# Performance work log

Measured on AMD Instinct MI355X. Metric: run time of the kernel, lower is better.

## Reference

```python
import jax, jax.numpy as jnp
import numpy as np

NUM_BINS = 8
TAIL = 3.0
MIN_W = 1e-3
MIN_H = 1e-3
MIN_D = 1e-3


def setup_inputs() -> dict:
    key = jax.random.key(0)
    k1, k2 = jax.random.split(key)
    inputs = jax.random.normal(k1, (8192, 2048), dtype=jnp.float32)
    params = 0.01 * jax.random.normal(k2, (2048, NUM_BINS * 3 - 1), dtype=jnp.float32)
    return {"inputs": inputs, "params": params}


def _rqs(inputs, params):
    # inputs: (B, D); params: (D, 3K-1). Each dim has its own spline (no coupling).
    K = NUM_BINS
    D = params.shape[0]
    uw = params[:, :K]
    uh = params[:, K:2 * K]
    ud = params[:, 2 * K:]  # (D, K-1)

    # pad edge derivatives so that softplus(const) = 1 - min_derivative (linear tails)
    const = float(np.log(np.exp(1.0 - MIN_D) - 1.0))
    ud = jnp.pad(ud, ((0, 0), (1, 1)), constant_values=const)  # (D, K+1)

    widths = MIN_W + (1.0 - MIN_W * K) * jax.nn.softmax(uw, axis=-1)
    cw = jnp.pad(jnp.cumsum(widths, axis=-1), ((0, 0), (1, 0)))  # (D, K+1) in [0,1]
    cw = (2.0 * TAIL) * cw - TAIL
    cw = cw.at[:, 0].set(-TAIL).at[:, -1].set(TAIL)
    widths = cw[:, 1:] - cw[:, :-1]

    heights = MIN_H + (1.0 - MIN_H * K) * jax.nn.softmax(uh, axis=-1)
    ch = jnp.pad(jnp.cumsum(heights, axis=-1), ((0, 0), (1, 0)))
    ch = (2.0 * TAIL) * ch - TAIL
    ch = ch.at[:, 0].set(-TAIL).at[:, -1].set(TAIL)
    heights = ch[:, 1:] - ch[:, :-1]

    derivs = MIN_D + jax.nn.softplus(ud)  # (D, K+1)

    inside = (inputs >= -TAIL) & (inputs <= TAIL)
    x = jnp.clip(inputs, -TAIL, TAIL)

    # searchsorted per element: bin index in [0, K-1], shape (B, D)
    idx = jnp.clip(jnp.sum((x[..., None] >= cw[None, :, :]).astype(jnp.int32), axis=-1) - 1, 0, K - 1)
    d_idx = jnp.arange(D)[None, :]  # broadcasts with (B, D) idx

    icw = cw[d_idx, idx]
    iw = widths[d_idx, idx]
    ich = ch[d_idx, idx]
    ih = heights[d_idx, idx]
    dlo = derivs[d_idx, idx]
    dhi = derivs[d_idx, idx + 1]

    delta = ih / iw
    theta = (x - icw) / iw
    t1m = theta * (1.0 - theta)

    numerator = ih * (delta * theta ** 2 + dlo * t1m)
    denominator = delta + (dlo + dhi - 2.0 * delta) * t1m
    out = ich + numerator / denominator

    deriv_num = delta ** 2 * (dhi * theta ** 2 + 2.0 * delta * t1m + dlo * (1.0 - theta) ** 2)
    logdet = jnp.log(deriv_num) - 2.0 * jnp.log(denominator)

    out = jnp.where(inside, out, inputs)     # identity tails
    logdet = jnp.where(inside, logdet, 0.0)
    return out, logdet


def reference(inputs, params):
    return _rqs(inputs, params)
```

## Files before the change

### kernel.cpp

```cpp
#include <hip/hip_runtime.h>


constexpr int   KBINS = 8;
constexpr float TAILF = 3.0f;
constexpr float MINW  = 0.001f;
constexpr float MINH  = 0.001f;
constexpr float MIND  = 0.001f;
constexpr int   NROWS = 8192;
constexpr int   NDIM  = 2048;
constexpr int   NPAR  = 3 * KBINS - 1;
constexpr int   VEC   = 2;
constexpr int   BLOCK = 256;
constexpr int   DIMS_PER_BLOCK = BLOCK * VEC;
constexpr int   BLOCKS_PER_ROW = NDIM / DIMS_PER_BLOCK;
constexpr int   GROWS = 512;
constexpr int   ROWS_PER_WALK = NROWS / GROWS;

typedef float v2f __attribute__((ext_vector_type(2)));

__device__ __forceinline__ float rcp_fast(float x) {
    return __builtin_amdgcn_rcpf(x);
}

__device__ __forceinline__ float softplus_fast(float x) {
    return fmaxf(x, 0.0f) + __logf(1.0f + __expf(-fabsf(x)));
}

__device__ __forceinline__ void build_tables(const float* __restrict__ p,
                                             float* cw, float* ch, float* dv,
                                             float edge_deriv) {
    {
        float u[KBINS];
        float m = p[0];
#pragma unroll
        for (int k = 1; k < KBINS; ++k) m = fmaxf(m, p[k]);
        float s = 0.0f;
#pragma unroll
        for (int k = 0; k < KBINS; ++k) { u[k] = __expf(p[k] - m); s += u[k]; }
        const float scale = (1.0f - MINW * KBINS) * rcp_fast(s);
        cw[0] = -TAILF;
        float acc = 0.0f;
#pragma unroll
        for (int k = 0; k < KBINS; ++k) {
            acc += MINW + scale * u[k];
            cw[k + 1] = fmaf(2.0f * TAILF, acc, -TAILF);
        }
        cw[KBINS] = TAILF;
    }
    {
        const float* q = p + KBINS;
        float u[KBINS];
        float m = q[0];
#pragma unroll
        for (int k = 1; k < KBINS; ++k) m = fmaxf(m, q[k]);
        float s = 0.0f;
#pragma unroll
        for (int k = 0; k < KBINS; ++k) { u[k] = __expf(q[k] - m); s += u[k]; }
        const float scale = (1.0f - MINH * KBINS) * rcp_fast(s);
        ch[0] = -TAILF;
        float acc = 0.0f;
#pragma unroll
        for (int k = 0; k < KBINS; ++k) {
            acc += MINH + scale * u[k];
            ch[k + 1] = fmaf(2.0f * TAILF, acc, -TAILF);
        }
        ch[KBINS] = TAILF;
    }
    dv[0] = edge_deriv;
    dv[KBINS] = edge_deriv;
#pragma unroll
    for (int k = 1; k < KBINS; ++k)
        dv[k] = MIND + softplus_fast(p[2 * KBINS + k - 1]);
}

__device__ __forceinline__ void rqs_eval(float x,
                                         const float* cw, const float* ch, const float* dv,
                                         float& o, float& ld) {
    const float xi = fminf(fmaxf(x, -TAILF), TAILF);
    float icw = cw[0], ncw = cw[1];
    float ich = ch[0], nch = ch[1];
    float dlo = dv[0], dhi = dv[1];
#pragma unroll
    for (int k = 1; k < KBINS; ++k) {
        const bool c = xi >= cw[k];
        icw = c ? cw[k]     : icw;
        ncw = c ? cw[k + 1] : ncw;
        ich = c ? ch[k]     : ich;
        nch = c ? ch[k + 1] : nch;
        dlo = c ? dv[k]     : dlo;
        dhi = c ? dv[k + 1] : dhi;
    }
    const float iw  = ncw - icw;
    const float ih  = nch - ich;
    const float riw = rcp_fast(iw);
    const float delta = ih * riw;
    const float theta = (xi - icw) * riw;
    const float omt   = 1.0f - theta;
    const float t1m   = theta * omt;
    const float th2   = theta * theta;
    const float num   = ih * fmaf(delta, th2, dlo * t1m);
    const float den   = fmaf(dlo + dhi - 2.0f * delta, t1m, delta);
    const float rden  = rcp_fast(den);
    const float o_in  = fmaf(num, rden, ich);
    const float dn    = (delta * delta) *
                        fmaf(dhi, th2, fmaf(2.0f * delta, t1m, dlo * (omt * omt)));
    const float ld_in = __logf(dn * rden * rden);
    const bool inside = (x >= -TAILF) && (x <= TAILF);
    o  = inside ? o_in : x;
    ld = inside ? ld_in : 0.0f;
}

__global__ __launch_bounds__(BLOCK, 4)
void rqs_kernel(const float* __restrict__ inp,
                const float* __restrict__ params,
                float* __restrict__ out) {
    const int b        = blockIdx.x;
    const int colBlock = b & (BLOCKS_PER_ROW - 1);
    const int rowGroup = b / BLOCKS_PER_ROW;
    const int d0   = colBlock * DIMS_PER_BLOCK + (int)threadIdx.x * VEC;
    const int row0 = rowGroup * ROWS_PER_WALK;

    const float edge_deriv = MIND + softplus_fast(__logf(__expf(1.0f - MIND) - 1.0f));

    float cw[VEC][KBINS + 1], ch[VEC][KBINS + 1], dv[VEC][KBINS + 1];
#pragma unroll
    for (int v = 0; v < VEC; ++v)
        build_tables(params + (size_t)(d0 + v) * NPAR, cw[v], ch[v], dv[v], edge_deriv);

    const v2f* __restrict__ in2 = (const v2f*)inp;
    v2f* __restrict__ out2 = (v2f*)out;
    v2f* __restrict__ ld2  = (v2f*)(out + (size_t)NROWS * NDIM);

    size_t idx2 = ((size_t)row0 * NDIM + d0) >> 1;
#pragma unroll 4
    for (int r = 0; r < ROWS_PER_WALK; ++r) {
        const v2f xv = in2[idx2];
        float o0, l0, o1, l1;
        rqs_eval(xv.x, cw[0], ch[0], dv[0], o0, l0);
        rqs_eval(xv.y, cw[1], ch[1], dv[1], o1, l1);
        v2f ov; ov.x = o0; ov.y = o1;
        v2f lv; lv.x = l0; lv.y = l1;
        out2[idx2] = ov;
        ld2[idx2]  = lv;
        idx2 += NDIM / 2;
    }
}

extern "C" void kernel_launch(void* const* d_in, const int* in_sizes, int n_in,
                              void* d_out, int out_size, void* d_ws, size_t ws_size,
                              hipStream_t stream) {
    const float* inp    = (const float*)d_in[0];
    const float* params = (const float*)d_in[1];
    float* out          = (float*)d_out;
    rqs_kernel<<<BLOCKS_PER_ROW * GROWS, BLOCK, 0, stream>>>(inp, params, out);
}
```

Measured before the change: 200.3 us.

## Move height/derivative tables to LDS and gather by computed bin index

```diff
diff --git a/kernel.cpp b/kernel.cpp
--- a/kernel.cpp
+++ b/kernel.cpp
@@ -26,70 +26,24 @@
     return fmaxf(x, 0.0f) + __logf(1.0f + __expf(-fabsf(x)));
 }
 
-__device__ __forceinline__ void build_tables(const float* __restrict__ p,
-                                             float* cw, float* ch, float* dv,
-                                             float edge_deriv) {
-    {
-        float u[KBINS];
-        float m = p[0];
-#pragma unroll
-        for (int k = 1; k < KBINS; ++k) m = fmaxf(m, p[k]);
-        float s = 0.0f;
-#pragma unroll
-        for (int k = 0; k < KBINS; ++k) { u[k] = __expf(p[k] - m); s += u[k]; }
-        const float scale = (1.0f - MINW * KBINS) * rcp_fast(s);
-        cw[0] = -TAILF;
-        float acc = 0.0f;
-#pragma unroll
-        for (int k = 0; k < KBINS; ++k) {
-            acc += MINW + scale * u[k];
-            cw[k + 1] = fmaf(2.0f * TAILF, acc, -TAILF);
-        }
-        cw[KBINS] = TAILF;
-    }
-    {
-        const float* q = p + KBINS;
-        float u[KBINS];
-        float m = q[0];
-#pragma unroll
-        for (int k = 1; k < KBINS; ++k) m = fmaxf(m, q[k]);
-        float s = 0.0f;
-#pragma unroll
-        for (int k = 0; k < KBINS; ++k) { u[k] = __expf(q[k] - m); s += u[k]; }
-        const float scale = (1.0f - MINH * KBINS) * rcp_fast(s);
-        ch[0] = -TAILF;
-        float acc = 0.0f;
-#pragma unroll
-        for (int k = 0; k < KBINS; ++k) {
-            acc += MINH + scale * u[k];
-            ch[k + 1] = fmaf(2.0f * TAILF, acc, -TAILF);
-        }
-        ch[KBINS] = TAILF;
-    }
-    dv[0] = edge_deriv;
-    dv[KBINS] = edge_deriv;
-#pragma unroll
-    for (int k = 1; k < KBINS; ++k)
-        dv[k] = MIND + softplus_fast(p[2 * KBINS + k - 1]);
-}
-
-__device__ __forceinline__ void rqs_eval(float x,
-                                         const float* cw, const float* ch, const float* dv,
+__device__ __forceinline__ void rqs_eval(float x, const float* __restrict__ cw,
+                                         const v2f* __restrict__ tab,
                                          float& o, float& ld) {
-    const float xi = fminf(fmaxf(x, -TAILF), TAILF);
+    const float xi = __builtin_amdgcn_fmed3f(x, -TAILF, TAILF);
     float icw = cw[0], ncw = cw[1];
-    float ich = ch[0], nch = ch[1];
-    float dlo = dv[0], dhi = dv[1];
+    int idx = 0;
 #pragma unroll
     for (int k = 1; k < KBINS; ++k) {
         const bool c = xi >= cw[k];
         icw = c ? cw[k]     : icw;
         ncw = c ? cw[k + 1] : ncw;
-        ich = c ? ch[k]     : ich;
-        nch = c ? ch[k + 1] : nch;
-        dlo = c ? dv[k]     : dlo;
-        dhi = c ? dv[k + 1] : dhi;
+        idx += c ? 1 : 0;
     }
+    const v2f lo = tab[idx];
+    const v2f hi = tab[idx + 1];
+    const float ich = lo.x, dlo = lo.y;
+    const float nch = hi.x, dhi = hi.y;
+
     const float iw  = ncw - icw;
     const float ih  = nch - ich;
     const float riw = rcp_fast(iw);
@@ -105,7 +59,7 @@
     const float dn    = (delta * delta) *
                         fmaf(dhi, th2, fmaf(2.0f * delta, t1m, dlo * (omt * omt)));
     const float ld_in = __logf(dn * rden * rden);
-    const bool inside = (x >= -TAILF) && (x <= TAILF);
+    const bool inside = fabsf(x) <= TAILF;
     o  = inside ? o_in : x;
     ld = inside ? ld_in : 0.0f;
 }
@@ -114,18 +68,68 @@
 void rqs_kernel(const float* __restrict__ inp,
                 const float* __restrict__ params,
                 float* __restrict__ out) {
+    __shared__ v2f chdv[DIMS_PER_BLOCK][KBINS + 1];
+
     const int b        = blockIdx.x;
     const int colBlock = b & (BLOCKS_PER_ROW - 1);
     const int rowGroup = b / BLOCKS_PER_ROW;
-    const int d0   = colBlock * DIMS_PER_BLOCK + (int)threadIdx.x * VEC;
+    const int l0   = (int)threadIdx.x * VEC;
+    const int d0   = colBlock * DIMS_PER_BLOCK + l0;
     const int row0 = rowGroup * ROWS_PER_WALK;
 
     const float edge_deriv = MIND + softplus_fast(__logf(__expf(1.0f - MIND) - 1.0f));
 
-    float cw[VEC][KBINS + 1], ch[VEC][KBINS + 1], dv[VEC][KBINS + 1];
+    float cw[VEC][KBINS + 1];
 #pragma unroll
-    for (int v = 0; v < VEC; ++v)
-        build_tables(params + (size_t)(d0 + v) * NPAR, cw[v], ch[v], dv[v], edge_deriv);
+    for (int v = 0; v < VEC; ++v) {
+        const float* __restrict__ p = params + (size_t)(d0 + v) * NPAR;
+        {
+            float u[KBINS];
+            float m = p[0];
+#pragma unroll
+            for (int k = 1; k < KBINS; ++k) m = fmaxf(m, p[k]);
+            float s = 0.0f;
+#pragma unroll
+            for (int k = 0; k < KBINS; ++k) { u[k] = __expf(p[k] - m); s += u[k]; }
+            const float scale = (1.0f - MINW * KBINS) * rcp_fast(s);
+            cw[v][0] = -TAILF;
+            float acc = 0.0f;
+#pragma unroll
+            for (int k = 0; k < KBINS - 1; ++k) {
+                acc += MINW + scale * u[k];
+                cw[v][k + 1] = fmaf(2.0f * TAILF, acc, -TAILF);
+            }
+            cw[v][KBINS] = TAILF;
+        }
+        {
+            const float* __restrict__ q = p + KBINS;
+            float u[KBINS];
+            float m = q[0];
+#pragma unroll
+            for (int k = 1; k < KBINS; ++k) m = fmaxf(m, q[k]);
+            float s = 0.0f;
+#pragma unroll
+            for (int k = 0; k < KBINS; ++k) { u[k] = __expf(q[k] - m); s += u[k]; }
+            const float scale = (1.0f - MINH * KBINS) * rcp_fast(s);
+            v2f e0; e0.x = -TAILF; e0.y = edge_deriv;
+            chdv[l0 + v][0] = e0;
+            float acc = 0.0f;
+#pragma unroll
+            for (int k = 0; k < KBINS; ++k) {
+                acc += MINH + scale * u[k];
+                v2f e;
+                e.x = (k == KBINS - 1) ? TAILF
+                                       : fmaf(2.0f * TAILF, acc, -TAILF);
+                e.y = (k == KBINS - 1) ? edge_deriv
+                                       : MIND + softplus_fast(p[2 * KBINS + k]);
+                chdv[l0 + v][k + 1] = e;
+            }
+        }
+    }
+    __syncthreads();
+
+    const v2f* __restrict__ tab0 = &chdv[l0][0];
+    const v2f* __restrict__ tab1 = &chdv[l0 + 1][0];
 
     const v2f* __restrict__ in2 = (const v2f*)inp;
     v2f* __restrict__ out2 = (v2f*)out;
@@ -135,11 +139,11 @@
 #pragma unroll 4
     for (int r = 0; r < ROWS_PER_WALK; ++r) {
         const v2f xv = in2[idx2];
-        float o0, l0, o1, l1;
-        rqs_eval(xv.x, cw[0], ch[0], dv[0], o0, l0);
-        rqs_eval(xv.y, cw[1], ch[1], dv[1], o1, l1);
+        float o0, ldv0, o1, ldv1;
+        rqs_eval(xv.x, cw[0], tab0, o0, ldv0);
+        rqs_eval(xv.y, cw[1], tab1, o1, ldv1);
         v2f ov; ov.x = o0; ov.y = o1;
-        v2f lv; lv.x = l0; lv.y = l1;
+        v2f lv; lv.x = ldv0; lv.y = ldv1;
         out2[idx2] = ov;
         ld2[idx2]  = lv;
         idx2 += NDIM / 2;
```

After: 199.4 us. About the same (-0.4%).
